# Performance work log

Hardware: AMD Instinct MI355X
Metric: run time of the kernel (lower is better)

## Reference

```python
import jax, jax.numpy as jnp
import numpy as np
from jax import lax

B, N, HID = 2, 2048, 2048
H, KVH, D = 16, 4, 128           # heads, kv heads, head_dim
GROUPS = H // KVH
FLA_WEIGHT = 0.01
NEG = -1e30


def setup_inputs() -> dict:
    key = jax.random.key(0)
    ks = jax.random.split(key, 5)
    s = 0.02
    return {
        "hidden_states": jax.random.normal(ks[0], (B, N, HID), jnp.float32),
        "Wq": jax.random.normal(ks[1], (HID, H * D), jnp.float32) * s,
        "Wk": jax.random.normal(ks[2], (HID, KVH * D), jnp.float32) * s,
        "Wv": jax.random.normal(ks[3], (HID, KVH * D), jnp.float32) * s,
        "Wo": jax.random.normal(ks[4], (H * D, HID), jnp.float32) * s,
    }


def _split_heads(x, h):
    b, n, _ = x.shape
    return x.reshape(b, n, h, -1).transpose(0, 2, 1, 3)  # b h n d


def _gla_attention(q, k, v, scale):
    # Gated linear attention: S_t = sigmoid(k_t) (.) S_{t-1} + k_t (x) v_t,
    # o_t = scale * q_t . S_t ; sequential recurrence over the seq dim.
    qs = jnp.moveaxis(q, 2, 0)  # n b h d
    ks = jnp.moveaxis(k, 2, 0)
    vs = jnp.moveaxis(v, 2, 0)

    def step(S, inp):
        qt, kt, vt = inp                                   # each (b,h,d)
        g = jax.nn.sigmoid(kt)                             # per-key-dim gate
        S = S * g[..., None] + kt[..., None] * vt[..., None, :]  # (b,h,d,dv)
        ot = scale * jnp.einsum('bhd,bhde->bhe', qt, S)
        return S, ot

    S0 = jnp.zeros(q.shape[:2] + (q.shape[-1], v.shape[-1]), q.dtype)
    _, o = lax.scan(step, S0, (qs, ks, vs))                # n b h dv
    return jnp.moveaxis(o, 0, 2)                           # b h n dv


def reference(hidden_states, Wq, Wk, Wv, Wo):
    scale = 1.0 / np.sqrt(D)
    q = _split_heads(hidden_states @ Wq, H)                # b h n d
    k = _split_heads(hidden_states @ Wk, KVH)
    v = _split_heads(hidden_states @ Wv, KVH)
    k = jnp.repeat(k, GROUPS, axis=1)                      # repeat_kv -> b H n d
    v = jnp.repeat(v, GROUPS, axis=1)

    # FLA branch
    fla = _gla_attention(q, k, v, scale)                   # b h n d
    fla = fla.transpose(0, 2, 1, 3).reshape(B, N, H * D)   # b n (h d)

    # Base causal softmax attention
    scores = jnp.einsum('bhnd,bhmd->bhnm', q, k) * scale
    causal = jnp.tril(jnp.ones((N, N), bool))
    scores = jnp.where(causal, scores, NEG)
    attn = jax.nn.softmax(scores, axis=-1)
    base = jnp.einsum('bhnm,bhmd->bhnd', attn, v)
    base = base.transpose(0, 2, 1, 3).reshape(B, N, H * D) @ Wo

    return base + FLA_WEIGHT * fla
```

## Files before the change

kernel.cpp:

```cpp
#include <hip/hip_runtime.h>
#include <hip/hip_bf16.h>
#include <cstdint>
#include <cstddef>


typedef __attribute__((ext_vector_type(4))) float f32x4;
typedef __attribute__((ext_vector_type(2))) float f32x2;
typedef __attribute__((ext_vector_type(8))) short s16x8;
typedef unsigned short u16;
typedef unsigned int u32;

__device__ __forceinline__ float bfu2f(u16 u) {
  union { unsigned int i; float f; } x; x.i = ((unsigned int)u) << 16; return x.f;
}
__device__ __forceinline__ u16 f2bfu(float f) {
  union { float f; unsigned int i; } x; x.f = f;
  unsigned int r = x.i + 0x7fffu + ((x.i >> 16) & 1u);
  return (u16)(r >> 16);
}
__device__ __forceinline__ void bf8_to_f(s16x8 v, float* o) {
  union { s16x8 v; u16 u[8]; } x; x.v = v;
#pragma unroll
  for (int j = 0; j < 8; j++) o[j] = bfu2f(x.u[j]);
}
__device__ __forceinline__ s16x8 pack_bf8(f32x4 lo, f32x4 hi) {
  union { s16x8 v; u16 u[8]; } x;
#pragma unroll
  for (int j = 0; j < 4; j++) { x.u[j] = f2bfu(lo[j]); x.u[4 + j] = f2bfu(hi[j]); }
  return x.v;
}
__device__ __forceinline__ void gload_lds16(const u16* g, u16* l) {
  __builtin_amdgcn_global_load_lds(
      (__attribute__((address_space(1))) void*)(g),
      (__attribute__((address_space(3))) void*)(l), 16, 0, 0);
}

__global__ __launch_bounds__(256) void f32_to_bf16(
    const float* __restrict__ src, u16* __restrict__ dst, int n8) {
  const int i = blockIdx.x * 256 + threadIdx.x;
  if (i < n8) {
    f32x4 a = *(const f32x4*)(src + (size_t)i * 8);
    f32x4 b = *(const f32x4*)(src + (size_t)i * 8 + 4);
    *(s16x8*)(dst + (size_t)i * 8) = pack_bf8(a, b);
  }
}

__global__ __launch_bounds__(256) void transpose_f32_bf16(
    const float* __restrict__ src, u16* __restrict__ dst, int R, int C) {
  __shared__ u16 tile[32][33];
  const int bx = blockIdx.x * 32, by = blockIdx.y * 32;
  const int tx = threadIdx.x & 31, ty = threadIdx.x >> 5;
#pragma unroll
  for (int i = 0; i < 32; i += 8)
    tile[ty + i][tx] = f2bfu(src[(size_t)(by + ty + i) * C + bx + tx]);
  __syncthreads();
#pragma unroll
  for (int i = 0; i < 32; i += 8)
    dst[(size_t)(bx + ty + i) * R + by + tx] = tile[tx][ty + i];
}

__global__ __launch_bounds__(256) void transpose_bf16(
    const u16* __restrict__ src, u16* __restrict__ dst, int R, int C) {
  __shared__ u16 tile[32][33];
  const int bx = blockIdx.x * 32, by = blockIdx.y * 32;
  const int tx = threadIdx.x & 31, ty = threadIdx.x >> 5;
#pragma unroll
  for (int i = 0; i < 32; i += 8)
    tile[ty + i][tx] = src[(size_t)(by + ty + i) * C + bx + tx];
  __syncthreads();
#pragma unroll
  for (int i = 0; i < 32; i += 8)
    dst[(size_t)(bx + ty + i) * R + by + tx] = tile[tx][ty + i];
}

__global__ __launch_bounds__(256) void gemm_t(
    const u16* __restrict__ A, const u16* __restrict__ Bt0, const u16* __restrict__ Bt1,
    u16* __restrict__ Cb0, u16* __restrict__ Cb1, float* __restrict__ Cf,
    int M, int N, int K, const u16* __restrict__ addsrc, float addw) {
  __shared__ u16 Al[128 * 32];
  __shared__ u16 Bl[128 * 32];
  const u16* Bt = blockIdx.z ? Bt1 : Bt0;
  u16* Cb = blockIdx.z ? Cb1 : Cb0;
  const int m0 = blockIdx.y * 128, n0 = blockIdx.x * 128;
  const int t = threadIdx.x, w = t >> 6, l = t & 63, lm = l & 15, lq = l >> 4;
  const int wr = w >> 1, wc = w & 1;
  const f32x4 z4 = {0.f, 0.f, 0.f, 0.f};
  f32x4 acc[4][4];
#pragma unroll
  for (int i = 0; i < 4; i++)
#pragma unroll
    for (int j = 0; j < 4; j++) acc[i][j] = z4;
  const int srow = l >> 2, scol = (l & 3) * 8;
  const u16* Ag = A + (size_t)(m0 + w * 32 + srow) * K + scol;
  const u16* Bg = Bt + (size_t)(n0 + w * 32 + srow) * K + scol;
  u16* Alw = &Al[(w * 32) * 32];
  u16* Blw = &Bl[(w * 32) * 32];
  for (int kk = 0; kk < K; kk += 32) {
    gload_lds16(Ag + kk, Alw);
    gload_lds16(Ag + (size_t)16 * K + kk, Alw + 16 * 32);
    gload_lds16(Bg + kk, Blw);
    gload_lds16(Bg + (size_t)16 * K + kk, Blw + 16 * 32);
    __syncthreads();
    s16x8 af[4], bfr[4];
#pragma unroll
    for (int sm = 0; sm < 4; sm++) af[sm] = *(const s16x8*)&Al[(wr * 64 + sm * 16 + lm) * 32 + lq * 8];
#pragma unroll
    for (int sn = 0; sn < 4; sn++) bfr[sn] = *(const s16x8*)&Bl[(wc * 64 + sn * 16 + lm) * 32 + lq * 8];
#pragma unroll
    for (int sm = 0; sm < 4; sm++)
#pragma unroll
      for (int sn = 0; sn < 4; sn++)
        acc[sm][sn] = __builtin_amdgcn_mfma_f32_16x16x32_bf16(af[sm], bfr[sn], acc[sm][sn], 0, 0, 0);
    __syncthreads();
  }
#pragma unroll
  for (int sm = 0; sm < 4; sm++)
#pragma unroll
    for (int sn = 0; sn < 4; sn++)
#pragma unroll
      for (int r = 0; r < 4; r++) {
        const int row = m0 + wr * 64 + sm * 16 + lq * 4 + r;
        const int col = n0 + wc * 64 + sn * 16 + lm;
        float v = acc[sm][sn][r];
        if (Cf) {
          if (addsrc) v += addw * bfu2f(addsrc[(size_t)row * N + col]);
          Cf[(size_t)row * N + col] = v;
        } else {
          Cb[(size_t)row * N + col] = f2bfu(v);
        }
      }
}

__global__ __launch_bounds__(512) void flash_attn_wave(
    const u16* __restrict__ Q, const u16* __restrict__ Kx,
    const u16* __restrict__ Vt, u16* __restrict__ AO) {
  __shared__ u16 Klds[64 * 128];
  __shared__ u16 Vlds[128 * 64];
  __shared__ u16 Pl[8][16][68];
  const int bid = blockIdx.x;
  const int set = bid & 7;
  const int b = set >> 2, kvh = set & 3;
  const int rest = bid >> 3;
  const int j0 = rest >> 1, hp = rest & 1;
  const int t = threadIdx.x, w = t >> 6, l = t & 63, lm = l & 15, lq = l >> 4;
  const int h = kvh * 4 + hp * 2 + (w & 1);
  const int cs = (w >> 1) & 1, mh = w >> 2;
  const float scale = 0.0883883476483184f;
  const u16* Kbase = Kx + (size_t)(b * 2048) * 512 + kvh * 128;
  const u16* Vbase = Vt + (size_t)(b * 512 + kvh * 128) * 2048;
  const f32x4 z4 = {0.f, 0.f, 0.f, 0.f};
  const char* KldsB = (const char*)Klds;
  const char* VldsB = (const char*)Vlds;

#pragma unroll 1
  for (int ph = 0; ph < 2; ph++) {
    const int j = ph ? (31 - j0) : j0;
    const int c = 2 * j + cs;
    const int base = c * 32;
    s16x8 qf[4];
#pragma unroll
    for (int kk = 0; kk < 4; kk++)
      qf[kk] = *(const s16x8*)(Q + ((size_t)(b * 2048 + base + mh * 16 + lm)) * 2048 +
                               h * 128 + kk * 32 + lq * 8);
    f32x4 oacc[8];
#pragma unroll
    for (int e = 0; e < 8; e++) oacc[e] = z4;
    float lsum[4] = {0.f, 0.f, 0.f, 0.f};
#pragma unroll 1
    for (int kt = 0; kt <= j; kt++) {
      const int key0 = kt * 64;
#pragma unroll
      for (int r = 0; r < 2; r++) {
        const int row = r * 32 + w * 4 + (l >> 4);
        const int cbyte = (l & 15) * 16;
        const int scb = cbyte ^ ((row & 7) << 4);
        gload_lds16(Kbase + (size_t)(key0 + row) * 512 + (scb >> 1),
                    Klds + r * 4096 + w * 512);
      }
#pragma unroll
      for (int r = 0; r < 2; r++) {
        const int row = r * 64 + w * 8 + (l >> 3);
        const int cbyte = (l & 7) * 16;
        const int scb = cbyte ^ ((row & 7) << 4);
        gload_lds16(Vbase + (size_t)row * 2048 + key0 + (scb >> 1),
                    Vlds + r * 4096 + w * 512);
      }
      __syncthreads();
      s16x8 kf[4][4];
#pragma unroll
      for (int nst = 0; nst < 4; nst++)
#pragma unroll
        for (int kk = 0; kk < 4; kk++) {
          const int row = nst * 16 + lm;
          const int cb = (kk * 64 + lq * 16) ^ ((row & 7) << 4);
          kf[nst][kk] = *(const s16x8*)(KldsB + row * 256 + cb);
        }
      f32x4 sacc[4];
#pragma unroll
      for (int i = 0; i < 4; i++) sacc[i] = z4;
#pragma unroll
      for (int nst = 0; nst < 4; nst++)
#pragma unroll
        for (int kk = 0; kk < 4; kk++)
          sacc[nst] = __builtin_amdgcn_mfma_f32_16x16x32_bf16(
              qf[kk], kf[nst][kk], sacc[nst], 0, 0, 0);
      const bool diag = (kt == j);
#pragma unroll
      for (int r = 0; r < 4; r++) {
        const int qrow = base + mh * 16 + lq * 4 + r;
#pragma unroll
        for (int nst = 0; nst < 4; nst++) {
          float pv = __expf(sacc[nst][r] * scale);
          if (diag && (key0 + nst * 16 + lm > qrow)) pv = 0.f;
          lsum[r] += pv;
          Pl[w][lq * 4 + r][nst * 16 + lm] = f2bfu(pv);
        }
      }
      s16x8 vf[8][2];
#pragma unroll
      for (int et = 0; et < 8; et++)
#pragma unroll
        for (int kc = 0; kc < 2; kc++) {
          const int row = et * 16 + lm;
          const int cb = (kc * 64 + lq * 16) ^ ((row & 7) << 4);
          vf[et][kc] = *(const s16x8*)(VldsB + row * 128 + cb);
        }
      s16x8 pf[2];
#pragma unroll
      for (int kc = 0; kc < 2; kc++)
        pf[kc] = *(const s16x8*)&Pl[w][lm][kc * 32 + lq * 8];
#pragma unroll
      for (int et = 0; et < 8; et++)
#pragma unroll
        for (int kc = 0; kc < 2; kc++)
          oacc[et] = __builtin_amdgcn_mfma_f32_16x16x32_bf16(
              pf[kc], vf[et][kc], oacc[et], 0, 0, 0);
      __syncthreads();
    }
#pragma unroll
    for (int r = 0; r < 4; r++) {
#pragma unroll
      for (int off = 1; off < 16; off <<= 1)
        lsum[r] += __shfl_xor(lsum[r], off, 64);
    }
#pragma unroll
    for (int r = 0; r < 4; r++) {
      const float inv = 1.f / lsum[r];
      const int row = base + mh * 16 + lq * 4 + r;
      u16* op = AO + ((size_t)(b * 2048 + row)) * 2048 + h * 128;
#pragma unroll
      for (int et = 0; et < 8; et++) op[et * 16 + lm] = f2bfu(oacc[et][r] * inv);
    }
  }
}

__global__ __launch_bounds__(256) void fla_contrib32(
    const u16* __restrict__ Kx, const u16* __restrict__ Vt,
    u16* __restrict__ Gg, u16* __restrict__ Ktg, u16* __restrict__ MT,
    float* __restrict__ Lam) {
  __shared__ float gl[32][132];
  __shared__ float kl[32][132];
  __shared__ float ktl[32][132];
  __shared__ u16 khT[128][40];
  const int c = blockIdx.x, kvh = blockIdx.y, b = blockIdx.z;
  const int bk = b * 4 + kvh;
  const int t = threadIdx.x;
  const size_t cb = (size_t)bk * 64 + c;
  {
    const int r = t >> 3, c0 = (t & 7) * 16;
    const u16* kp = Kx + ((size_t)(b * 2048 + c * 32 + r)) * 512 + kvh * 128 + c0;
#pragma unroll
    for (int i = 0; i < 2; i++) {
      float kv[8];
      bf8_to_f(*(const s16x8*)(kp + i * 8), kv);
#pragma unroll
      for (int j = 0; j < 8; j++) {
        kl[r][c0 + i * 8 + j] = kv[j];
        gl[r][c0 + i * 8 + j] = 1.f / (1.f + __expf(-kv[j]));
      }
    }
  }
  __syncthreads();
  if (t < 128) {
    float G = 1.f;
#pragma unroll
    for (int s = 0; s < 32; s++) {
      G *= gl[s][t];
      gl[s][t] = G;
      ktl[s][t] = kl[s][t] / G;
    }
    Lam[cb * 128 + t] = G;
    const float lam = G;
#pragma unroll
    for (int s = 0; s < 32; s++) khT[t][s] = f2bfu(ktl[s][t] * lam);
  }
  __syncthreads();
  {
    const int r = t >> 3, c0 = (t & 7) * 16;
    u16* gp = Gg + cb * 4096 + r * 128 + c0;
    u16* kp = Ktg + cb * 4096 + r * 128 + c0;
#pragma unroll
    for (int i = 0; i < 2; i++) {
      f32x4 a = *(f32x4*)&gl[r][c0 + i * 8];
      f32x4 b2 = *(f32x4*)&gl[r][c0 + i * 8 + 4];
      *(s16x8*)(gp + i * 8) = pack_bf8(a, b2);
      a = *(f32x4*)&ktl[r][c0 + i * 8];
      b2 = *(f32x4*)&ktl[r][c0 + i * 8 + 4];
      *(s16x8*)(kp + i * 8) = pack_bf8(a, b2);
    }
  }
  const int w = t >> 6, l = t & 63, lm = l & 15, lq = l >> 4;
  const f32x4 z4 = {0.f, 0.f, 0.f, 0.f};
  f32x4 macc[2][8];
#pragma unroll
  for (int ei = 0; ei < 2; ei++)
#pragma unroll
    for (int dt = 0; dt < 8; dt++) macc[ei][dt] = z4;
  s16x8 vtf[2];
#pragma unroll
  for (int ei = 0; ei < 2; ei++) {
    const int et = w * 2 + ei;
    vtf[ei] = *(const s16x8*)(Vt + ((size_t)(b * 512 + kvh * 128 + et * 16 + lm)) * 2048 +
                              c * 32 + lq * 8);
  }
#pragma unroll
  for (int dt = 0; dt < 8; dt++) {
    s16x8 kf = *(const s16x8*)&khT[dt * 16 + lm][lq * 8];
#pragma unroll
    for (int ei = 0; ei < 2; ei++)
      macc[ei][dt] = __builtin_amdgcn_mfma_f32_16x16x32_bf16(vtf[ei], kf, macc[ei][dt], 0, 0, 0);
  }
  u16* mp = MT + cb * 16384;
#pragma unroll
  for (int ei = 0; ei < 2; ei++)
#pragma unroll
    for (int dt = 0; dt < 8; dt++)
#pragma unroll
      for (int r = 0; r < 4; r++)
        mp[(size_t)((w * 2 + ei) * 16 + lq * 4 + r) * 128 + dt * 16 + lm] =
            f2bfu(macc[ei][dt][r]);
}

__global__ __launch_bounds__(256) void fla_prefix32(
    const u16* __restrict__ MT, const float* __restrict__ Lam, u16* __restrict__ SwsT) {
  const int eg = blockIdx.x, bk = blockIdx.y;
  const int t = threadIdx.x;
  const int e = eg * 4 + (t >> 6), d0 = (t & 63) * 2;
  const size_t cb0 = (size_t)bk * 64;
  const u16* mp = MT + cb0 * 16384 + e * 128 + d0;
  const float* lp = Lam + cb0 * 128 + d0;
  u16* sp = SwsT + cb0 * 16384 + e * 128 + d0;
  float s0 = 0.f, s1 = 0.f;
  u32 mnext = *(const u32*)mp;
  f32x2 lnext = *(const f32x2*)lp;
#pragma unroll 1
  for (int c = 0; c < 64; c++) {
    const u32 mcur = mnext;
    const f32x2 lcur = lnext;
    if (c < 63) {
      mnext = *(const u32*)(mp + (size_t)(c + 1) * 16384);
      lnext = *(const f32x2*)(lp + (size_t)(c + 1) * 128);
    }
    *(u32*)(sp + (size_t)c * 16384) = (u32)f2bfu(s0) | ((u32)f2bfu(s1) << 16);
    s0 = s0 * lcur[0] + bfu2f((u16)(mcur & 0xffffu));
    s1 = s1 * lcur[1] + bfu2f((u16)(mcur >> 16));
  }
}

__global__ __launch_bounds__(256) void fla_output_mfma(
    const u16* __restrict__ Q, const u16* __restrict__ Gg, const u16* __restrict__ Ktg,
    const u16* __restrict__ SwsT, const u16* __restrict__ Vt, u16* __restrict__ Fla) {
  __shared__ u16 Pl[4][2][16][40];
  const int c = blockIdx.x, h = blockIdx.y, b = blockIdx.z;
  const int kvh = h >> 2, bk = b * 4 + kvh;
  const int t = threadIdx.x, w = t >> 6, l = t & 63, lm = l & 15, lq = l >> 4;
  const float scale = 0.0883883476483184f;
  const size_t cb = (size_t)bk * 64 + c;
  const f32x4 z4 = {0.f, 0.f, 0.f, 0.f};
  s16x8 qgf[2][4];
#pragma unroll
  for (int m = 0; m < 2; m++)
#pragma unroll
    for (int kk = 0; kk < 4; kk++) {
      float qv[8], gv[8];
      bf8_to_f(*(const s16x8*)(Q + ((size_t)(b * 2048 + c * 32 + m * 16 + lm)) * 2048 +
                               h * 128 + kk * 32 + lq * 8), qv);
      bf8_to_f(*(const s16x8*)(Gg + cb * 4096 + (m * 16 + lm) * 128 + kk * 32 + lq * 8), gv);
      f32x4 a, b2;
#pragma unroll
      for (int j = 0; j < 4; j++) { a[j] = qv[j] * gv[j]; b2[j] = qv[4 + j] * gv[4 + j]; }
      qgf[m][kk] = pack_bf8(a, b2);
    }
  f32x4 sacc[2][2];
#pragma unroll
  for (int m = 0; m < 2; m++)
#pragma unroll
    for (int st = 0; st < 2; st++) sacc[m][st] = z4;
#pragma unroll
  for (int st = 0; st < 2; st++)
#pragma unroll
    for (int kk = 0; kk < 4; kk++) {
      s16x8 ktf = *(const s16x8*)(Ktg + cb * 4096 + (st * 16 + lm) * 128 + kk * 32 + lq * 8);
#pragma unroll
      for (int m = 0; m < 2; m++)
        sacc[m][st] = __builtin_amdgcn_mfma_f32_16x16x32_bf16(qgf[m][kk], ktf, sacc[m][st], 0, 0, 0);
    }
#pragma unroll
  for (int m = 0; m < 2; m++)
#pragma unroll
    for (int st = 0; st < 2; st++)
#pragma unroll
      for (int r = 0; r < 4; r++) {
        const int trow = m * 16 + lq * 4 + r;
        const int scol = st * 16 + lm;
        Pl[w][m][lq * 4 + r][st * 16 + lm] = f2bfu(scol <= trow ? sacc[m][st][r] : 0.f);
      }
  s16x8 pf[2];
#pragma unroll
  for (int m = 0; m < 2; m++) pf[m] = *(const s16x8*)&Pl[w][m][lm][lq * 8];
  f32x4 oacc[2][2];
#pragma unroll
  for (int m = 0; m < 2; m++)
#pragma unroll
    for (int ei = 0; ei < 2; ei++) oacc[m][ei] = z4;
#pragma unroll
  for (int ei = 0; ei < 2; ei++) {
    const int et = w * 2 + ei;
    s16x8 vtf = *(const s16x8*)(Vt + ((size_t)(b * 512 + kvh * 128 + et * 16 + lm)) * 2048 +
                                c * 32 + lq * 8);
#pragma unroll
    for (int m = 0; m < 2; m++)
      oacc[m][ei] = __builtin_amdgcn_mfma_f32_16x16x32_bf16(pf[m], vtf, oacc[m][ei], 0, 0, 0);
#pragma unroll
    for (int kk = 0; kk < 4; kk++) {
      s16x8 s0f = *(const s16x8*)(SwsT + cb * 16384 + (et * 16 + lm) * 128 + kk * 32 + lq * 8);
#pragma unroll
      for (int m = 0; m < 2; m++)
        oacc[m][ei] = __builtin_amdgcn_mfma_f32_16x16x32_bf16(qgf[m][kk], s0f, oacc[m][ei], 0, 0, 0);
    }
  }
#pragma unroll
  for (int m = 0; m < 2; m++)
#pragma unroll
    for (int ei = 0; ei < 2; ei++)
#pragma unroll
      for (int r = 0; r < 4; r++)
        Fla[((size_t)(b * 2048 + c * 32 + m * 16 + lq * 4 + r)) * 2048 + h * 128 +
            (w * 2 + ei) * 16 + lm] = f2bfu(scale * oacc[m][ei][r]);
}

extern "C" void kernel_launch(void* const* d_in, const int* in_sizes, int n_in,
                              void* d_out, int out_size, void* d_ws, size_t ws_size,
                              hipStream_t stream) {
  const float* X  = (const float*)d_in[0];
  const float* Wq = (const float*)d_in[1];
  const float* Wk = (const float*)d_in[2];
  const float* Wv = (const float*)d_in[3];
  const float* Wo = (const float*)d_in[4];
  float* out = (float*)d_out;

  char* ws = (char*)d_ws;
  size_t off = 0;
  auto alloc = [&](size_t bytes) { void* p = ws + off; off += (bytes + 255) & ~(size_t)255; return p; };
  u16* WoT = (u16*)alloc(2048ull * 2048 * 2);
  u16* Qb  = (u16*)alloc(4096ull * 2048 * 2);
  u16* Kb  = (u16*)alloc(4096ull * 512 * 2);
  u16* Vb  = (u16*)alloc(4096ull * 512 * 2);
  u16* Vtb = (u16*)alloc(2ull * 512 * 2048 * 2);
  u16* Fla = (u16*)alloc(4096ull * 2048 * 2);
  u16* SH16 = (u16*)alloc(4096ull * 2048 * 2);
  u16* Xb = SH16;
  u16* MT = SH16;
  u16* AO = SH16;
  char* BIG = (char*)alloc(26ull * 1024 * 1024);
  u16* WqT = (u16*)BIG;
  u16* WkT = (u16*)(BIG + 8ull * 1024 * 1024);
  u16* WvT = (u16*)(BIG + 10ull * 1024 * 1024);
  u16* Gg   = (u16*)BIG;
  u16* Ktg  = (u16*)(BIG + 4194304ull);
  u16* SwsT = (u16*)(BIG + 8388608ull);
  float* Lam = (float*)(BIG + 8388608ull + 16777216ull);
  (void)ws_size; (void)in_sizes; (void)n_in; (void)out_size;

  dim3 blk(256);
  f32_to_bf16<<<dim3(4096), blk, 0, stream>>>(X, Xb, 4096 * 2048 / 8);
  transpose_f32_bf16<<<dim3(64, 64), blk, 0, stream>>>(Wq, WqT, 2048, 2048);
  transpose_f32_bf16<<<dim3(16, 64), blk, 0, stream>>>(Wk, WkT, 2048, 512);
  transpose_f32_bf16<<<dim3(16, 64), blk, 0, stream>>>(Wv, WvT, 2048, 512);
  transpose_f32_bf16<<<dim3(64, 64), blk, 0, stream>>>(Wo, WoT, 2048, 2048);

  gemm_t<<<dim3(16, 32, 1), blk, 0, stream>>>(Xb, WqT, WqT, Qb, Qb, nullptr,
                                              4096, 2048, 2048, nullptr, 0.f);
  gemm_t<<<dim3(4, 32, 2), blk, 0, stream>>>(Xb, WkT, WvT, Kb, Vb, nullptr,
                                             4096, 512, 2048, nullptr, 0.f);

  transpose_bf16<<<dim3(16, 64), blk, 0, stream>>>(Vb, Vtb, 2048, 512);
  transpose_bf16<<<dim3(16, 64), blk, 0, stream>>>(Vb + 2048ull * 512, Vtb + 512ull * 2048, 2048, 512);

  fla_contrib32<<<dim3(64, 4, 2), blk, 0, stream>>>(Kb, Vtb, Gg, Ktg, MT, Lam);
  fla_prefix32<<<dim3(32, 8), blk, 0, stream>>>(MT, Lam, SwsT);
  fla_output_mfma<<<dim3(64, 16, 2), blk, 0, stream>>>(Qb, Gg, Ktg, SwsT, Vtb, Fla);

  flash_attn_wave<<<dim3(256), dim3(512), 0, stream>>>(Qb, Kb, Vtb, AO);

  gemm_t<<<dim3(16, 32, 1), blk, 0, stream>>>(AO, WoT, WoT, nullptr, nullptr, out,
                                              4096, 2048, 2048, Fla, 0.01f);
}
```

Measured before the change: 430.5 us.

## Double-buffer K/V tiles in flash attention and fuse Q/K/V projection GEMMs

The flash attention kernel now keeps two LDS buffers for K and V. It prefetches the next key tile while computing on the current one, using explicit vmcnt waits and raw barriers in place of __syncthreads. This aims to hide global-load latency behind the MFMA work. Separately, the Q and K/V projection GEMMs are merged into one launch of 24x32 blocks that pick their weight and output by block index, which removes one launch and balances the grid. The double buffer doubles the K/V LDS use, which may lower occupancy, and the hand-written waitcnt values have to match the number of loads issued.

```diff
diff --git a/kernel.cpp b/kernel.cpp
--- a/kernel.cpp
+++ b/kernel.cpp
@@ -131,11 +131,67 @@
       }
 }
 
+__global__ __launch_bounds__(256) void gemm_qkv(
+    const u16* __restrict__ A, const u16* __restrict__ WqT, const u16* __restrict__ WkT,
+    const u16* __restrict__ WvT, u16* __restrict__ Qo, u16* __restrict__ Ko,
+    u16* __restrict__ Vo) {
+  __shared__ u16 Al[128 * 32];
+  __shared__ u16 Bl[128 * 32];
+  const int bx = blockIdx.x;
+  const u16* Bt; u16* Cb; int n0, Nst;
+  if (bx < 16)      { Bt = WqT; Cb = Qo; n0 = bx * 128;        Nst = 2048; }
+  else if (bx < 20) { Bt = WkT; Cb = Ko; n0 = (bx - 16) * 128; Nst = 512; }
+  else              { Bt = WvT; Cb = Vo; n0 = (bx - 20) * 128; Nst = 512; }
+  const int K = 2048;
+  const int m0 = blockIdx.y * 128;
+  const int t = threadIdx.x, w = t >> 6, l = t & 63, lm = l & 15, lq = l >> 4;
+  const int wr = w >> 1, wc = w & 1;
+  const f32x4 z4 = {0.f, 0.f, 0.f, 0.f};
+  f32x4 acc[4][4];
+#pragma unroll
+  for (int i = 0; i < 4; i++)
+#pragma unroll
+    for (int j = 0; j < 4; j++) acc[i][j] = z4;
+  const int srow = l >> 2, scol = (l & 3) * 8;
+  const u16* Ag = A + (size_t)(m0 + w * 32 + srow) * K + scol;
+  const u16* Bg = Bt + (size_t)(n0 + w * 32 + srow) * K + scol;
+  u16* Alw = &Al[(w * 32) * 32];
+  u16* Blw = &Bl[(w * 32) * 32];
+  for (int kk = 0; kk < K; kk += 32) {
+    gload_lds16(Ag + kk, Alw);
+    gload_lds16(Ag + (size_t)16 * K + kk, Alw + 16 * 32);
+    gload_lds16(Bg + kk, Blw);
+    gload_lds16(Bg + (size_t)16 * K + kk, Blw + 16 * 32);
+    __syncthreads();
+    s16x8 af[4], bfr[4];
+#pragma unroll
+    for (int sm = 0; sm < 4; sm++) af[sm] = *(const s16x8*)&Al[(wr * 64 + sm * 16 + lm) * 32 + lq * 8];
+#pragma unroll
+    for (int sn = 0; sn < 4; sn++) bfr[sn] = *(const s16x8*)&Bl[(wc * 64 + sn * 16 + lm) * 32 + lq * 8];
+#pragma unroll
+    for (int sm = 0; sm < 4; sm++)
+#pragma unroll
+      for (int sn = 0; sn < 4; sn++)
+        acc[sm][sn] = __builtin_amdgcn_mfma_f32_16x16x32_bf16(af[sm], bfr[sn], acc[sm][sn], 0, 0, 0);
+    __syncthreads();
+  }
+#pragma unroll
+  for (int sm = 0; sm < 4; sm++)
+#pragma unroll
+    for (int sn = 0; sn < 4; sn++)
+#pragma unroll
+      for (int r = 0; r < 4; r++) {
+        const int row = m0 + wr * 64 + sm * 16 + lq * 4 + r;
+        const int col = n0 + wc * 64 + sn * 16 + lm;
+        Cb[(size_t)row * Nst + col] = f2bfu(acc[sm][sn][r]);
+      }
+}
+
 __global__ __launch_bounds__(512) void flash_attn_wave(
     const u16* __restrict__ Q, const u16* __restrict__ Kx,
     const u16* __restrict__ Vt, u16* __restrict__ AO) {
-  __shared__ u16 Klds[64 * 128];
-  __shared__ u16 Vlds[128 * 64];
+  __shared__ u16 Klds[2][64 * 128];
+  __shared__ u16 Vlds[2][128 * 64];
   __shared__ u16 Pl[8][16][68];
   const int bid = blockIdx.x;
   const int set = bid & 7;
@@ -149,14 +205,36 @@
   const u16* Kbase = Kx + (size_t)(b * 2048) * 512 + kvh * 128;
   const u16* Vbase = Vt + (size_t)(b * 512 + kvh * 128) * 2048;
   const f32x4 z4 = {0.f, 0.f, 0.f, 0.f};
-  const char* KldsB = (const char*)Klds;
-  const char* VldsB = (const char*)Vlds;
+
+  const int kdst0 = w * 512, kdst1 = 4096 + w * 512;
+  const int krow_a = (l >> 4), kcol_sw = (((l & 15) * 16)) >> 1;
+  (void)krow_a; (void)kcol_sw;
+
+  auto stage = [&](int kt, int bufi) {
+    const int key0 = kt * 64;
+#pragma unroll
+    for (int r = 0; r < 2; r++) {
+      const int row = r * 32 + w * 4 + (l >> 4);
+      const int scb = ((l & 15) * 16) ^ ((row & 7) << 4);
+      gload_lds16(Kbase + (size_t)(key0 + row) * 512 + (scb >> 1),
+                  &Klds[bufi][r * 4096 + w * 512]);
+    }
+#pragma unroll
+    for (int r = 0; r < 2; r++) {
+      const int row = r * 64 + w * 8 + (l >> 3);
+      const int scb = ((l & 7) * 16) ^ ((row & 7) << 4);
+      gload_lds16(Vbase + (size_t)row * 2048 + key0 + (scb >> 1),
+                  &Vlds[bufi][r * 4096 + w * 512]);
+    }
+  };
 
 #pragma unroll 1
   for (int ph = 0; ph < 2; ph++) {
     const int j = ph ? (31 - j0) : j0;
     const int c = 2 * j + cs;
     const int base = c * 32;
+    int cur = 0;
+    stage(0, 0);
     s16x8 qf[4];
 #pragma unroll
     for (int kk = 0; kk < 4; kk++)
@@ -169,23 +247,15 @@
 #pragma unroll 1
     for (int kt = 0; kt <= j; kt++) {
       const int key0 = kt * 64;
-#pragma unroll
-      for (int r = 0; r < 2; r++) {
-        const int row = r * 32 + w * 4 + (l >> 4);
-        const int cbyte = (l & 15) * 16;
-        const int scb = cbyte ^ ((row & 7) << 4);
-        gload_lds16(Kbase + (size_t)(key0 + row) * 512 + (scb >> 1),
-                    Klds + r * 4096 + w * 512);
+      if (kt < j) {
+        stage(kt + 1, cur ^ 1);
+        asm volatile("s_waitcnt vmcnt(4)" ::: "memory");
+      } else {
+        asm volatile("s_waitcnt vmcnt(0)" ::: "memory");
       }
-#pragma unroll
-      for (int r = 0; r < 2; r++) {
-        const int row = r * 64 + w * 8 + (l >> 3);
-        const int cbyte = (l & 7) * 16;
-        const int scb = cbyte ^ ((row & 7) << 4);
-        gload_lds16(Vbase + (size_t)row * 2048 + key0 + (scb >> 1),
-                    Vlds + r * 4096 + w * 512);
-      }
-      __syncthreads();
+      __builtin_amdgcn_s_barrier();
+      const char* KB = (const char*)&Klds[cur][0];
+      const char* VB = (const char*)&Vlds[cur][0];
       s16x8 kf[4][4];
 #pragma unroll
       for (int nst = 0; nst < 4; nst++)
@@ -193,7 +263,7 @@
         for (int kk = 0; kk < 4; kk++) {
           const int row = nst * 16 + lm;
           const int cb = (kk * 64 + lq * 16) ^ ((row & 7) << 4);
-          kf[nst][kk] = *(const s16x8*)(KldsB + row * 256 + cb);
+          kf[nst][kk] = *(const s16x8*)(KB + row * 256 + cb);
         }
       f32x4 sacc[4];
 #pragma unroll
@@ -223,7 +293,7 @@
         for (int kc = 0; kc < 2; kc++) {
           const int row = et * 16 + lm;
           const int cb = (kc * 64 + lq * 16) ^ ((row & 7) << 4);
-          vf[et][kc] = *(const s16x8*)(VldsB + row * 128 + cb);
+          vf[et][kc] = *(const s16x8*)(VB + row * 128 + cb);
         }
       s16x8 pf[2];
 #pragma unroll
@@ -235,7 +305,9 @@
         for (int kc = 0; kc < 2; kc++)
           oacc[et] = __builtin_amdgcn_mfma_f32_16x16x32_bf16(
               pf[kc], vf[et][kc], oacc[et], 0, 0, 0);
-      __syncthreads();
+      asm volatile("s_waitcnt lgkmcnt(0)" ::: "memory");
+      __builtin_amdgcn_s_barrier();
+      cur ^= 1;
     }
 #pragma unroll
     for (int r = 0; r < 4; r++) {
@@ -489,10 +561,7 @@
   transpose_f32_bf16<<<dim3(16, 64), blk, 0, stream>>>(Wv, WvT, 2048, 512);
   transpose_f32_bf16<<<dim3(64, 64), blk, 0, stream>>>(Wo, WoT, 2048, 2048);
 
-  gemm_t<<<dim3(16, 32, 1), blk, 0, stream>>>(Xb, WqT, WqT, Qb, Qb, nullptr,
-                                              4096, 2048, 2048, nullptr, 0.f);
-  gemm_t<<<dim3(4, 32, 2), blk, 0, stream>>>(Xb, WkT, WvT, Kb, Vb, nullptr,
-                                             4096, 512, 2048, nullptr, 0.f);
+  gemm_qkv<<<dim3(24, 32), blk, 0, stream>>>(Xb, WqT, WkT, WvT, Qb, Kb, Vb);
 
   transpose_bf16<<<dim3(16, 64), blk, 0, stream>>>(Vb, Vtb, 2048, 512);
   transpose_bf16<<<dim3(16, 64), blk, 0, stream>>>(Vb + 2048ull * 512, Vtb + 512ull * 2048, 2048, 512);
```

After: 384.7 us. -10.6%, faster.
